# Kernel optimization log

Hardware: AMD Instinct MI355X
Metric: run time of the kernel (lower is better)

The kernel has to match this reference:

```python
import jax, jax.numpy as jnp
import numpy as np

EPS = 1e-5

def _layernorm(x, g, b):
    mu = jnp.mean(x, axis=-1, keepdims=True)
    var = jnp.mean(jnp.square(x - mu), axis=-1, keepdims=True)
    return (x - mu) * jax.lax.rsqrt(var + EPS) * g + b

def _silu(x):
    return x * jax.nn.sigmoid(x)

def _xavier(key, shape):
    fan_out, fan_in = shape
    limit = np.sqrt(6.0 / (fan_in + fan_out))
    return jax.random.uniform(key, shape, jnp.float32, -limit, limit)

def setup_inputs() -> dict:
    key = jax.random.key(0)
    ks = jax.random.split(key, 4)
    B = 2097152
    return {
        'x': jax.random.normal(ks[0], (B, 24), jnp.float32),
        'w1': _xavier(ks[1], (64, 24)), 'b1': jnp.zeros((64,), jnp.float32),
        'g1': jnp.ones((64,), jnp.float32), 'be1': jnp.zeros((64,), jnp.float32),
        'w2': _xavier(ks[2], (64, 64)), 'b2': jnp.zeros((64,), jnp.float32),
        'g2': jnp.ones((64,), jnp.float32), 'be2': jnp.zeros((64,), jnp.float32),
        'w3': _xavier(ks[3], (7, 64)), 'b3': jnp.zeros((7,), jnp.float32),
        'g3': jnp.ones((7,), jnp.float32), 'be3': jnp.zeros((7,), jnp.float32),
    }

def reference(x, w1, b1, g1, be1, w2, b2, g2, be2, w3, b3, g3, be3):
    h = _silu(_layernorm(x @ w1.T + b1, g1, be1))      # [B, 64]
    h = _silu(_layernorm(h @ w2.T + b2, g2, be2))      # [B, 64]
    h = _layernorm(h @ w3.T + b3, g3, be3)             # [B, 7]
    return jax.nn.softmax(h, axis=-1)
```

## Files before the change

### kernel.cpp

```cpp
#include <hip/hip_runtime.h>
#include <math.h>

#define BLOCK 256
#define WPB 4
#define NBLOCKS 2048

typedef float  f32x4 __attribute__((ext_vector_type(4)));
typedef float  f32x2 __attribute__((ext_vector_type(2)));
typedef short  short8 __attribute__((ext_vector_type(8)));
typedef unsigned int u32;
typedef u32 u32x4 __attribute__((ext_vector_type(4)));
typedef u32 u32x2 __attribute__((ext_vector_type(2)));

static __device__ __forceinline__ f32x4 mfma16(short8 a, short8 b, f32x4 c) {
    return __builtin_amdgcn_mfma_f32_16x16x32_bf16(a, b, c, 0, 0, 0);
}

static __device__ __forceinline__ f32x4 zero4() { f32x4 z = {0.f, 0.f, 0.f, 0.f}; return z; }

static __device__ __forceinline__ u32 cvt_pk(float lo, float hi) {
    u32 r;
    asm("v_cvt_pk_bf16_f32 %0, %1, %2" : "=v"(r) : "v"(lo), "v"(hi));
    return r;
}
static __device__ __forceinline__ float unpk_lo(u32 p) { return __builtin_bit_cast(float, p << 16); }
static __device__ __forceinline__ float unpk_hi(u32 p) { return __builtin_bit_cast(float, p & 0xffff0000u); }

static __device__ __forceinline__ short8 mk_frag(u32 a, u32 b, u32 c, u32 d) {
    u32x4 t = {a, b, c, d};
    return __builtin_bit_cast(short8, t);
}

struct Frag2 { short8 hi, lo; };

static __device__ __forceinline__ Frag2 split8(f32x4 a, f32x4 b) {
    u32 h0 = cvt_pk(a[0], a[1]), h1 = cvt_pk(a[2], a[3]);
    u32 h2 = cvt_pk(b[0], b[1]), h3 = cvt_pk(b[2], b[3]);
    u32 l0 = cvt_pk(a[0] - unpk_lo(h0), a[1] - unpk_hi(h0));
    u32 l1 = cvt_pk(a[2] - unpk_lo(h1), a[3] - unpk_hi(h1));
    u32 l2 = cvt_pk(b[0] - unpk_lo(h2), b[1] - unpk_hi(h2));
    u32 l3 = cvt_pk(b[2] - unpk_lo(h3), b[3] - unpk_hi(h3));
    Frag2 r; r.hi = mk_frag(h0, h1, h2, h3); r.lo = mk_frag(l0, l1, l2, l3);
    return r;
}

static __device__ __forceinline__ void split4(f32x4 v, u32x2& hi, u32x2& lo) {
    u32 h0 = cvt_pk(v[0], v[1]), h1 = cvt_pk(v[2], v[3]);
    u32 l0 = cvt_pk(v[0] - unpk_lo(h0), v[1] - unpk_hi(h0));
    u32 l1 = cvt_pk(v[2] - unpk_lo(h1), v[3] - unpk_hi(h1));
    hi = u32x2{h0, h1}; lo = u32x2{l0, l1};
}

static __device__ __forceinline__ Frag2 wfrag(const float* p) {
    return split8(*(const f32x4*)p, *(const f32x4*)(p + 4));
}

static __device__ __forceinline__ float red4(float v) {
    v += __shfl_xor(v, 16);
    v += __shfl_xor(v, 32);
    return v;
}
static __device__ __forceinline__ float redmax4(float v) {
    v = fmaxf(v, __shfl_xor(v, 16));
    v = fmaxf(v, __shfl_xor(v, 32));
    return v;
}

struct TState {
    f32x4 xa, xb;
    f32x4 d[4];
    short8 bhHi[2], bhLo[2];
    f32x4 d3;
};

static __device__ __forceinline__ void ph_l1(TState& t, const Frag2& bx, const Frag2* w1f) {
#pragma unroll
    for (int mt = 0; mt < 4; ++mt) {
        f32x4 d = mfma16(w1f[mt].hi, bx.hi, zero4());
        d = mfma16(w1f[mt].hi, bx.lo, d);
        d = mfma16(w1f[mt].lo, bx.hi, d);
        t.d[mt] = d;
    }
}

static __device__ __forceinline__ void ph_l2_lds(TState& t,
        const unsigned char* sW2h, const unsigned char* sW2l, u32 crow, u32 ch, int q) {
    const u32 r0 = crow + ((((u32)q) ^ ch) << 4);
    const u32 r1 = crow + ((((u32)(4 + q)) ^ ch) << 4);
#pragma unroll
    for (int mt = 0; mt < 4; ++mt) {
        const u32 mo = (u32)mt * 2048u;
        short8 h0 = *(const short8*)(sW2h + mo + r0);
        short8 h1 = *(const short8*)(sW2h + mo + r1);
        short8 l0 = *(const short8*)(sW2l + mo + r0);
        short8 l1 = *(const short8*)(sW2l + mo + r1);
        f32x4 d = mfma16(h0, t.bhHi[0], zero4());
        d = mfma16(h0, t.bhLo[0], d);
        d = mfma16(l0, t.bhHi[0], d);
        d = mfma16(h1, t.bhHi[1], d);
        d = mfma16(h1, t.bhLo[1], d);
        d = mfma16(l1, t.bhHi[1], d);
        t.d[mt] = d;
    }
}

static __device__ __forceinline__ void ph_l3_lds(TState& t,
        const unsigned char* sW3h, const unsigned char* sW3l, u32 crow, u32 ch, int q) {
    const u32 r0 = crow + ((((u32)q) ^ ch) << 4);
    const u32 r1 = crow + ((((u32)(4 + q)) ^ ch) << 4);
    short8 h0 = *(const short8*)(sW3h + r0);
    short8 h1 = *(const short8*)(sW3h + r1);
    short8 l0 = *(const short8*)(sW3l + r0);
    short8 l1 = *(const short8*)(sW3l + r1);
    f32x4 a = mfma16(h0, t.bhHi[0], zero4());
    a = mfma16(h0, t.bhLo[0], a);
    a = mfma16(l0, t.bhHi[0], a);
    f32x4 b = mfma16(h1, t.bhHi[1], zero4());
    b = mfma16(h1, t.bhLo[1], b);
    b = mfma16(l1, t.bhHi[1], b);
    t.d3 = a + b;
}

template<int PB, int PG, int PBE>
static __device__ __forceinline__ void ph_ln_silu(TState& t, const float* sP, int q) {
    if (PB >= 0) {
#pragma unroll
        for (int mt = 0; mt < 4; ++mt)
            t.d[mt] += *(const f32x4*)(sP + PB + mt * 16 + q * 4);
    }
    f32x4 acc  = (t.d[0] + t.d[1]) + (t.d[2] + t.d[3]);
    f32x4 acc2 = t.d[0] * t.d[0];
    acc2 += t.d[1] * t.d[1];
    acc2 += t.d[2] * t.d[2];
    acc2 += t.d[3] * t.d[3];
    float s  = (acc[0] + acc[1]) + (acc[2] + acc[3]);
    float s2 = (acc2[0] + acc2[1]) + (acc2[2] + acc2[3]);
    s = red4(s); s2 = red4(s2);
    const float mu = s * (1.f / 64.f);
    const float var = s2 * (1.f / 64.f) - mu * mu;
    const float inv = __builtin_amdgcn_rsqf(var + 1e-5f);
    const float cns = -mu * inv;
#pragma unroll
    for (int mt = 0; mt < 4; ++mt) {
        const f32x4 gv  = *(const f32x4*)(sP + PG  + mt * 16 + q * 4);
        const f32x4 bev = *(const f32x4*)(sP + PBE + mt * 16 + q * 4);
        f32x4 tt = t.d[mt] * inv + cns;
        f32x4 v  = tt * gv + bev;
        f32x4 sg;
#pragma unroll
        for (int r = 0; r < 4; ++r)
            sg[r] = __builtin_amdgcn_rcpf(1.f + __expf(-v[r]));
        t.d[mt] = v * sg;
    }
}

static __device__ __forceinline__ void ph_stage(TState& t, unsigned char* sHi, unsigned char* sLo,
                                                u32 crow, u32 ch, int q) {
#pragma unroll
    for (int mt = 0; mt < 4; ++mt) {
        u32x2 hi, lo;
        split4(t.d[mt], hi, lo);
        u32 off = crow + ((((u32)(mt * 2 + (q >> 1))) ^ ch) << 4) + (u32)((q & 1) * 8);
        *(u32x2*)(sHi + off) = hi;
        *(u32x2*)(sLo + off) = lo;
    }
#pragma unroll
    for (int kk = 0; kk < 2; ++kk) {
        u32 roff = crow + ((((u32)(kk * 4 + q)) ^ ch) << 4);
        t.bhHi[kk] = *(const short8*)(sHi + roff);
        t.bhLo[kk] = *(const short8*)(sLo + roff);
    }
}

static __device__ __forceinline__ void ph_out(TState& t, const float* sP, int q, int c, int lane,
                                              unsigned char* ob, float* out, int tile,
                                              int oc0, int of0, int oc1, int of1) {
    const f32x4 b3v  = *(const f32x4*)(sP + 384 + q * 4);
    const f32x4 g3v  = *(const f32x4*)(sP + 400 + q * 4);
    const f32x4 be3v = *(const f32x4*)(sP + 416 + q * 4);
    f32x4 d3 = t.d3 + b3v;
    float s = 0.f, s2 = 0.f;
#pragma unroll
    for (int r = 0; r < 4; ++r) {
        const bool ok = (q * 4 + r) < 7;
        if (ok) { s += d3[r]; s2 = fmaf(d3[r], d3[r], s2); }
    }
    s = red4(s); s2 = red4(s2);
    const float mu = s * (1.f / 7.f);
    const float var = s2 * (1.f / 7.f) - mu * mu;
    const float inv = __builtin_amdgcn_rsqf(var + 1e-5f);
    const float cns = -mu * inv;

    f32x4 z = (d3 * inv + cns) * g3v + be3v;
    float mx = -1e30f;
#pragma unroll
    for (int r = 0; r < 4; ++r) {
        const bool ok = (q * 4 + r) < 7;
        if (ok) mx = fmaxf(mx, z[r]);
    }
    mx = redmax4(mx);
    float es = 0.f; float e[4];
#pragma unroll
    for (int r = 0; r < 4; ++r) {
        const bool ok = (q * 4 + r) < 7;
        e[r] = ok ? __expf(z[r] - mx) : 0.f;
        es += e[r];
    }
    es = red4(es);
    const float rs = __builtin_amdgcn_rcpf(es);

    if (q == 0) {
        f32x4 v = {e[0] * rs, e[1] * rs, e[2] * rs, e[3] * rs};
        *(f32x4*)(ob + c * 48) = v;
    } else if (q == 1) {
        f32x2 v = {e[0] * rs, e[1] * rs};
        *(f32x2*)(ob + c * 48 + 16) = v;
        *(float*)(ob + c * 48 + 24) = e[2] * rs;
    }
    float* outp = out + (size_t)tile * 112;
    outp[lane] = *(const float*)(ob + oc0 * 48 + of0 * 4);
    if (lane < 48) outp[64 + lane] = *(const float*)(ob + oc1 * 48 + of1 * 4);
}

__global__ __launch_bounds__(BLOCK, 4) void mlp_mfma5_kernel(
    const float* __restrict__ x,
    const float* __restrict__ w1, const float* __restrict__ b1,
    const float* __restrict__ g1, const float* __restrict__ be1,
    const float* __restrict__ w2, const float* __restrict__ b2,
    const float* __restrict__ g2, const float* __restrict__ be2,
    const float* __restrict__ w3, const float* __restrict__ b3,
    const float* __restrict__ g3, const float* __restrict__ be3,
    float* __restrict__ out, int ntiles)
{
    __shared__ __align__(16) unsigned char smem[WPB * 4096 + 16384 + 4096];
    __shared__ __align__(16) float sP[6 * 64 + 3 * 16];

    const int tid = threadIdx.x;
    const int lane = tid & 63;
    const int wib  = tid >> 6;
    const int c = lane & 15;
    const int q = lane >> 4;

    unsigned char* wb   = smem + wib * 4096;
    unsigned char* sHi  = wb;
    unsigned char* sLo  = wb + 2048;
    unsigned char* ob   = sHi;
    unsigned char* sW2h = smem + WPB * 4096;
    unsigned char* sW2l = sW2h + 8192;
    unsigned char* sW3h = sW2l + 8192;
    unsigned char* sW3l = sW3h + 2048;

    for (int i = tid; i < 512; i += BLOCK) {
        const int row = i >> 3, cb = i & 7;
        Frag2 f = wfrag(w2 + row * 64 + cb * 8);
        const u32 off = (u32)row * 128u + (u32)((cb ^ (row & 7)) << 4);
        *(short8*)(sW2h + off) = f.hi;
        *(short8*)(sW2l + off) = f.lo;
    }
    if (tid < 128) {
        const int row = tid >> 3, cb = tid & 7;
        Frag2 f;
        if (row < 7) f = wfrag(w3 + row * 64 + cb * 8);
        else         { f.hi = mk_frag(0,0,0,0); f.lo = mk_frag(0,0,0,0); }
        const u32 off = (u32)row * 128u + (u32)((cb ^ (row & 7)) << 4);
        *(short8*)(sW3h + off) = f.hi;
        *(short8*)(sW3l + off) = f.lo;
    }
    if (tid < 64) {
        sP[        tid] = b1[tid];  sP[ 64 + tid] = g1[tid];  sP[128 + tid] = be1[tid];
        sP[192 + tid] = b2[tid];    sP[256 + tid] = g2[tid];  sP[320 + tid] = be2[tid];
    }
    if (tid < 16) {
        const bool ok = tid < 7;
        sP[384 + tid] = ok ? b3[tid]  : 0.f;
        sP[400 + tid] = ok ? g3[tid]  : 0.f;
        sP[416 + tid] = ok ? be3[tid] : 0.f;
    }

    const u32 crow = (u32)c * 128u;
    const u32 ch   = (u32)(c & 7);

    Frag2 w1f[4];
#pragma unroll
    for (int mt = 0; mt < 4; ++mt) {
        if (q < 3) {
            w1f[mt] = wfrag(w1 + (mt * 16 + c) * 24 + q * 8);
        } else {
            float s = b1[mt * 16 + c];
            f32x4 a = {s, 0.f, 0.f, 0.f};
            w1f[mt] = split8(a, zero4());
        }
    }

    __syncthreads();

    const int oc0 = lane / 7, of0 = lane - oc0 * 7;
    const int i1 = lane + 64;
    const int oc1 = i1 / 7, of1 = i1 - oc1 * 7;

    const int wid = blockIdx.x * WPB + wib;
    const int ts  = gridDim.x * WPB;

    TState A;
    A.xa = zero4(); A.xb = zero4();
    if (wid < ntiles && q < 3) {
        const float* xp = x + ((size_t)wid * 16 + c) * 24 + q * 8;
        A.xa = *(const f32x4*)xp; A.xb = *(const f32x4*)(xp + 4);
    }
    if (q == 3) A.xa[0] = 1.0f;

    for (int tile = wid; tile < ntiles; tile += ts) {
        asm volatile("" ::: "memory");

        Frag2 bx = split8(A.xa, A.xb);

        {
            const int nt = tile + ts;
            if (nt < ntiles && q < 3) {
                const float* xp = x + ((size_t)nt * 16 + c) * 24 + q * 8;
                A.xa = *(const f32x4*)xp; A.xb = *(const f32x4*)(xp + 4);
            }
        }

        ph_l1(A, bx, w1f);
        ph_ln_silu<-1, 64, 128>(A, sP, q);
        ph_stage(A, sHi, sLo, crow, ch, q);
        ph_l2_lds(A, sW2h, sW2l, crow, ch, q);
        ph_ln_silu<192, 256, 320>(A, sP, q);
        ph_stage(A, sHi, sLo, crow, ch, q);
        ph_l3_lds(A, sW3h, sW3l, crow, ch, q);
        ph_out(A, sP, q, c, lane, ob, out, tile, oc0, of0, oc1, of1);
    }
}

extern "C" void kernel_launch(void* const* d_in, const int* in_sizes, int n_in,
                              void* d_out, int out_size, void* d_ws, size_t ws_size,
                              hipStream_t stream) {
    const float* x   = (const float*)d_in[0];
    const float* w1  = (const float*)d_in[1];
    const float* b1  = (const float*)d_in[2];
    const float* g1  = (const float*)d_in[3];
    const float* be1 = (const float*)d_in[4];
    const float* w2  = (const float*)d_in[5];
    const float* b2  = (const float*)d_in[6];
    const float* g2  = (const float*)d_in[7];
    const float* be2 = (const float*)d_in[8];
    const float* w3  = (const float*)d_in[9];
    const float* b3  = (const float*)d_in[10];
    const float* g3  = (const float*)d_in[11];
    const float* be3 = (const float*)d_in[12];
    float* out = (float*)d_out;

    const int B = in_sizes[0] / 24;
    const int ntiles = B / 16;
    hipLaunchKernelGGL(mlp_mfma5_kernel, dim3(NBLOCKS), dim3(BLOCK), 0, stream,
                       x, w1, b1, g1, be1, w2, b2, g2, be2, w3, b3, g3, be3,
                       out, ntiles);
}
```

Before: 183.5 us.

## Interleave two independent tiles per wave and relax launch bounds

Each wave now processes two tiles per loop iteration, A and B, with their phases interleaved so MFMA, LDS and transcendental latency of one tile can overlap with the other. Input prefetch is extended to two tiles ahead. The output store is guarded for the possibly out-of-range second tile. The launch-bounds occupancy hint drops from 4 to 3 blocks per CU to leave room for the extra register state, trading occupancy for instruction-level parallelism.

```diff
diff --git a/kernel.cpp b/kernel.cpp
--- a/kernel.cpp
+++ b/kernel.cpp
@@ -173,7 +173,7 @@
 }
 
 static __device__ __forceinline__ void ph_out(TState& t, const float* sP, int q, int c, int lane,
-                                              unsigned char* ob, float* out, int tile,
+                                              unsigned char* ob, float* out, int tile, bool valid,
                                               int oc0, int of0, int oc1, int of1) {
     const f32x4 b3v  = *(const f32x4*)(sP + 384 + q * 4);
     const f32x4 g3v  = *(const f32x4*)(sP + 400 + q * 4);
@@ -217,12 +217,14 @@
         *(f32x2*)(ob + c * 48 + 16) = v;
         *(float*)(ob + c * 48 + 24) = e[2] * rs;
     }
-    float* outp = out + (size_t)tile * 112;
-    outp[lane] = *(const float*)(ob + oc0 * 48 + of0 * 4);
-    if (lane < 48) outp[64 + lane] = *(const float*)(ob + oc1 * 48 + of1 * 4);
-}
-
-__global__ __launch_bounds__(BLOCK, 4) void mlp_mfma5_kernel(
+    if (valid) {
+        float* outp = out + (size_t)tile * 112;
+        outp[lane] = *(const float*)(ob + oc0 * 48 + of0 * 4);
+        if (lane < 48) outp[64 + lane] = *(const float*)(ob + oc1 * 48 + of1 * 4);
+    }
+}
+
+__global__ __launch_bounds__(BLOCK, 3) void mlp_mfma7_kernel(
     const float* __restrict__ x,
     const float* __restrict__ w1, const float* __restrict__ b1,
     const float* __restrict__ g1, const float* __restrict__ be1,
@@ -301,35 +303,53 @@
     const int wid = blockIdx.x * WPB + wib;
     const int ts  = gridDim.x * WPB;
 
-    TState A;
-    A.xa = zero4(); A.xb = zero4();
-    if (wid < ntiles && q < 3) {
-        const float* xp = x + ((size_t)wid * 16 + c) * 24 + q * 8;
-        A.xa = *(const f32x4*)xp; A.xb = *(const f32x4*)(xp + 4);
-    }
-    if (q == 3) A.xa[0] = 1.0f;
-
-    for (int tile = wid; tile < ntiles; tile += ts) {
+    TState A, B;
+    A.xa = zero4(); A.xb = zero4(); B.xa = zero4(); B.xb = zero4();
+    {
+        const int t0 = wid, t1 = wid + ts;
+        if (t0 < ntiles && q < 3) {
+            const float* xp = x + ((size_t)t0 * 16 + c) * 24 + q * 8;
+            A.xa = *(const f32x4*)xp; A.xb = *(const f32x4*)(xp + 4);
+        }
+        if (t1 < ntiles && q < 3) {
+            const float* xp = x + ((size_t)t1 * 16 + c) * 24 + q * 8;
+            B.xa = *(const f32x4*)xp; B.xb = *(const f32x4*)(xp + 4);
+        }
+        if (q == 3) { A.xa[0] = 1.0f; B.xa[0] = 1.0f; }
+    }
+
+    for (int tile = wid; tile < ntiles; tile += 2 * ts) {
         asm volatile("" ::: "memory");
 
-        Frag2 bx = split8(A.xa, A.xb);
+        const int tB = tile + ts;
+        const bool vB = tB < ntiles;
+
+        Frag2 bxA = split8(A.xa, A.xb);
+        Frag2 bxB = split8(B.xa, B.xb);
 
         {
-            const int nt = tile + ts;
-            if (nt < ntiles && q < 3) {
-                const float* xp = x + ((size_t)nt * 16 + c) * 24 + q * 8;
+            const int tA2 = tile + 2 * ts, tB2 = tile + 3 * ts;
+            if (tA2 < ntiles && q < 3) {
+                const float* xp = x + ((size_t)tA2 * 16 + c) * 24 + q * 8;
                 A.xa = *(const f32x4*)xp; A.xb = *(const f32x4*)(xp + 4);
             }
+            if (tB2 < ntiles && q < 3) {
+                const float* xp = x + ((size_t)tB2 * 16 + c) * 24 + q * 8;
+                B.xa = *(const f32x4*)xp; B.xb = *(const f32x4*)(xp + 4);
+            }
         }
 
-        ph_l1(A, bx, w1f);
-        ph_ln_silu<-1, 64, 128>(A, sP, q);
-        ph_stage(A, sHi, sLo, crow, ch, q);
+        ph_l1(A, bxA, w1f);                  ph_l1(B, bxB, w1f);
+        ph_ln_silu<-1, 64, 128>(A, sP, q);   ph_ln_silu<-1, 64, 128>(B, sP, q);
+        ph_stage(A, sHi, sLo, crow, ch, q);  ph_stage(B, sHi, sLo, crow, ch, q);
         ph_l2_lds(A, sW2h, sW2l, crow, ch, q);
-        ph_ln_silu<192, 256, 320>(A, sP, q);
-        ph_stage(A, sHi, sLo, crow, ch, q);
+        ph_l2_lds(B, sW2h, sW2l, crow, ch, q);
+        ph_ln_silu<192, 256, 320>(A, sP, q); ph_ln_silu<192, 256, 320>(B, sP, q);
+        ph_stage(A, sHi, sLo, crow, ch, q);  ph_stage(B, sHi, sLo, crow, ch, q);
         ph_l3_lds(A, sW3h, sW3l, crow, ch, q);
-        ph_out(A, sP, q, c, lane, ob, out, tile, oc0, of0, oc1, of1);
+        ph_l3_lds(B, sW3h, sW3l, crow, ch, q);
+        ph_out(A, sP, q, c, lane, ob, out, tile, true, oc0, of0, oc1, of1);
+        ph_out(B, sP, q, c, lane, ob, out, tB,   vB,   oc0, of0, oc1, of1);
     }
 }
 
@@ -352,8 +372,8 @@
     float* out = (float*)d_out;
 
     const int B = in_sizes[0] / 24;
-    const int ntiles = B / 16;
-    hipLaunchKernelGGL(mlp_mfma5_kernel, dim3(NBLOCKS), dim3(BLOCK), 0, stream,
+    const int nt = B / 16;
+    hipLaunchKernelGGL(mlp_mfma7_kernel, dim3(NBLOCKS), dim3(BLOCK), 0, stream,
                        x, w1, b1, g1, be1, w2, b2, g2, be2, w3, b3, g3, be3,
-                       out, ntiles);
-}
+                       out, nt);
+}
```

Measured after the change: 185.2 us. Within noise of the previous version (+1.0%).
